# Optimization experiments

Measured on AMD Instinct MI355X. Metric: run time of the kernel, lower is better.

Reference implementation:

```python
import jax, jax.numpy as jnp
import numpy as np

DIM = 512   # feature channels (dim)
K = 3       # depthwise kernel size
H = 256     # grid extent along pos[:,0]
W = 256     # grid extent along pos[:,1]
N = 20000   # number of occupied spots (unique coordinates)


def setup_inputs() -> dict:
    key = jax.random.key(0)
    k1, k2, k3 = jax.random.split(key, 3)
    rng = np.random.default_rng(0)
    # N unique flat cells; pin corners so the dense grid extent is exactly HxW
    flat = np.concatenate([[0, H * W - 1], rng.permutation(H * W - 2)[: N - 2] + 1])
    pos = jnp.asarray(np.stack([flat // W, flat % W], axis=1), dtype=jnp.int32)  # (N,2)
    x = jax.random.normal(k1, (1, N, DIM), jnp.float32)
    weight = jax.random.normal(k2, (DIM, 1, K, K), jnp.float32) * 0.05  # depthwise OIHW
    bias = jax.random.normal(k3, (DIM,), jnp.float32) * 0.05
    return {"x": x, "pos": pos, "weight": weight, "bias": bias}


def reference(x, pos, weight, bias):
    pos = pos - pos.min(axis=0)                 # shift to origin (as torch)
    p0, p1 = pos[:, 0], pos[:, 1]
    xsq = x[0]                                  # (N, DIM)
    # scatter sparse coords to dense grid (duplicates would sum, coords unique)
    grid = jnp.zeros((H, W, DIM), x.dtype).at[p0, p1].add(xsq)   # (H, W, DIM)
    xd = grid.transpose(2, 1, 0)[None]          # (1, DIM, W, H) == permute(2,1,0).unsqueeze(0)
    conv = jax.lax.conv_general_dilated(
        xd, weight, (1, 1), "SAME",
        dimension_numbers=("NCHW", "OIHW", "NCHW"),
        feature_group_count=DIM,
    ) + bias[None, :, None, None]
    mask = xd.sum(axis=1, keepdims=True) != 0.0  # occupied cells
    out_d = jnp.where(mask, conv, 0.0) + xd      # masked residual
    dense = out_d[0].transpose(2, 1, 0)          # (H, W, DIM)
    # gather back to sparse values; torch to_sparse(2) orders rows lexicographically
    order = jnp.lexsort((p1, p0))
    vals = dense[p0[order], p1[order]]           # (N, DIM)
    return vals[None]                            # (1, N, DIM)
```

## Files before the change

### kernel.cpp

```cpp
#include <hip/hip_runtime.h>

#define HH 256
#define WW 256
#define DIM 512

typedef float f32x4 __attribute__((ext_vector_type(4)));


__global__ __launch_bounds__(256) void scatter_kernel(const int* __restrict__ pos,
                                                      int* __restrict__ cell_map,
                                                      int n) {
    int i = blockIdx.x * 256 + threadIdx.x;
    if (i >= n) return;
    int p0 = pos[2 * i];
    int p1 = pos[2 * i + 1];
    cell_map[p0 * WW + p1] = i;
}

__global__ __launch_bounds__(256) void rank_kernel(const int* __restrict__ cell_map,
                                                   int* __restrict__ sorted) {
    __shared__ int red[256];
    __shared__ int wt[4];
    const int t = threadIdx.x;
    const int b = blockIdx.x;
    const int limit = b * 256;

    int cnt = 0;
    const int4* cm4 = (const int4*)cell_map;
    for (int i = t; i * 4 < limit; i += 256) {
        int4 v = cm4[i];
        cnt += (v.x >= 0) + (v.y >= 0) + (v.z >= 0) + (v.w >= 0);
    }
    red[t] = cnt;
    __syncthreads();
    #pragma unroll
    for (int d = 128; d > 0; d >>= 1) {
        if (t < d) red[t] += red[t + d];
        __syncthreads();
    }
    int blk_off = red[0];

    int cell = limit + t;
    int m = cell_map[cell];
    bool occ = (m >= 0);
    unsigned long long mask = __ballot(occ);
    int lane = t & 63;
    int wave = t >> 6;
    int pre = __popcll(mask & ((1ull << lane) - 1ull));
    if (lane == 0) wt[wave] = __popcll(mask);
    __syncthreads();
    int woff = 0;
    for (int i = 0; i < wave; ++i) woff += wt[i];
    if (occ) sorted[blk_off + woff + pre] = (m << 16) | cell;
}

__global__ __launch_bounds__(256, 6) void conv_main(const float* __restrict__ x,
                                                    const float* __restrict__ weight,
                                                    const float* __restrict__ bias,
                                                    const int* __restrict__ cell_map,
                                                    const int* __restrict__ sorted,
                                                    float* __restrict__ out,
                                                    int n) {
    const int lane = threadIdx.x & 63;
    const int wv   = threadIdx.x >> 6;

    const int nb  = gridDim.x;
    const int cid = (blockIdx.x & 7) * (nb >> 3) + (blockIdx.x >> 3);
    const int T   = 2 * n;
    const int ppb = (T + nb - 1) / nb;
    const int base = cid * ppb;
    int endt = base + ppb; if (endt > T) endt = T;

    int t = base + wv;
    if (t >= endt) return;

    const int hf = t & 1;
    const int c0 = hf * (DIM / 2) + lane * 4;

    float wtv[36];
    {
        const float4* wb = (const float4*)(weight + c0 * 9);
        #pragma unroll
        for (int q = 0; q < 9; ++q) {
            float4 v = wb[q];
            wtv[4 * q + 0] = v.x; wtv[4 * q + 1] = v.y;
            wtv[4 * q + 2] = v.z; wtv[4 * q + 3] = v.w;
        }
    }
    float bj[4];
    {
        float4 b0 = *(const float4*)(bias + c0);
        bj[0]=b0.x; bj[1]=b0.y; bj[2]=b0.z; bj[3]=b0.w;
    }
    #pragma unroll
    for (int j = 0; j < 4; ++j) wtv[j * 9 + 4] += 1.0f;

    int pk = __builtin_amdgcn_readfirstlane(sorted[t >> 1]);

    while (t < endt) {
        const int tn = t + 4;
        int pk_next = 0;
        if (tn < endt)
            pk_next = __builtin_amdgcn_readfirstlane(sorted[tn >> 1]);

        const int p    = pk >> 16;
        const int flat = pk & 0xFFFF;
        const int h = flat >> 8;
        const int w = flat & (WW - 1);

        int m[9];
        #pragma unroll
        for (int k = 0; k < 9; ++k) {
            if (k == 4) { m[4] = -1; continue; }
            int dh = k % 3 - 1;
            int dw = k / 3 - 1;
            int hh = h + dh;
            int ww = w + dw;
            int v = -1;
            if ((unsigned)hh < (unsigned)HH && (unsigned)ww < (unsigned)WW)
                v = cell_map[hh * WW + ww];
            m[k] = __builtin_amdgcn_readfirstlane(v);
        }

        const float* xs = x + (size_t)p * DIM + c0;
        float4 s0 = *(const float4*)(xs);
        float acc[4];
        acc[0] = bj[0] + s0.x * wtv[0*9+4];
        acc[1] = bj[1] + s0.y * wtv[1*9+4];
        acc[2] = bj[2] + s0.z * wtv[2*9+4];
        acc[3] = bj[3] + s0.w * wtv[3*9+4];

        #pragma unroll
        for (int k = 0; k < 9; ++k) {
            if (k == 4) continue;
            if (m[k] >= 0) {
                const float* xn = x + (size_t)m[k] * DIM + c0;
                float4 n0 = *(const float4*)(xn);
                acc[0] += n0.x * wtv[0*9+k];
                acc[1] += n0.y * wtv[1*9+k];
                acc[2] += n0.z * wtv[2*9+k];
                acc[3] += n0.w * wtv[3*9+k];
            }
        }

        const int r = t >> 1;
        float* op = out + (size_t)r * DIM + c0;
        f32x4 o0 = { acc[0], acc[1], acc[2], acc[3] };
        __builtin_nontemporal_store(o0, (f32x4*)op);

        t = tn;
        pk = pk_next;
    }
}

extern "C" void kernel_launch(void* const* d_in, const int* in_sizes, int n_in,
                              void* d_out, int out_size, void* d_ws, size_t ws_size,
                              hipStream_t stream) {
    const float* x      = (const float*)d_in[0];
    const int*   pos    = (const int*)d_in[1];
    const float* weight = (const float*)d_in[2];
    const float* bias   = (const float*)d_in[3];
    float* out = (float*)d_out;

    int n = in_sizes[1] / 2;

    int* ws       = (int*)d_ws;
    int* cell_map = ws;
    int* sorted   = ws + HH * WW;

    scatter_kernel<<<(n + 255) / 256, 256, 0, stream>>>(pos, cell_map, n);
    rank_kernel<<<256, 256, 0, stream>>>(cell_map, sorted);

    const int nblocks = 1536;
    conv_main<<<nblocks, 256, 0, stream>>>(x, weight, bias, cell_map, sorted, out, n);
}
```

Before: 129.2 us.

## Software-pipeline neighbor lookup and use branchless zero-row loads in conv

The conv loop now resolves the next point's nine neighbor indices from cell_map while the current point's feature loads are in flight. It also replaces conditional neighbor loads with unconditional loads that point at a zeroed row, which scatter_kernel initialises in the workspace. Launch bounds go from 6 to 4 blocks per CU and the grid shrinks from 1536 to 1024 blocks to leave room for the extra registers. The cost is always issuing eight neighbor loads, including ones that only read zeros, plus more register pressure and lower occupancy.

```diff
diff --git a/kernel.cpp b/kernel.cpp
--- a/kernel.cpp
+++ b/kernel.cpp
@@ -9,7 +9,12 @@
 
 __global__ __launch_bounds__(256) void scatter_kernel(const int* __restrict__ pos,
                                                       int* __restrict__ cell_map,
+                                                      float* __restrict__ zrow,
                                                       int n) {
+    if (blockIdx.x == 0) {
+        float2 z = {0.0f, 0.0f};
+        ((float2*)zrow)[threadIdx.x] = z;
+    }
     int i = blockIdx.x * 256 + threadIdx.x;
     if (i >= n) return;
     int p0 = pos[2 * i];
@@ -54,20 +59,38 @@
     if (occ) sorted[blk_off + woff + pre] = (m << 16) | cell;
 }
 
-__global__ __launch_bounds__(256, 6) void conv_main(const float* __restrict__ x,
+__device__ __forceinline__ void resolve9(const int* __restrict__ cm, int pk, int* m) {
+    const int h = (pk >> 8) & 255;
+    const int w = pk & 255;
+    #pragma unroll
+    for (int k = 0; k < 9; ++k) {
+        if (k == 4) { m[4] = -1; continue; }
+        int dh = k % 3 - 1;
+        int dw = k / 3 - 1;
+        int hh = h + dh;
+        int ww = w + dw;
+        bool ok = ((hh | ww) & ~255) == 0;
+        int cl = ok ? hh * WW + ww : 0;
+        int v  = cm[cl];
+        m[k]   = ok ? v : -1;
+    }
+}
+
+__global__ __launch_bounds__(256, 4) void conv_main(const float* __restrict__ x,
                                                     const float* __restrict__ weight,
                                                     const float* __restrict__ bias,
                                                     const int* __restrict__ cell_map,
                                                     const int* __restrict__ sorted,
+                                                    const float* __restrict__ zrow,
                                                     float* __restrict__ out,
                                                     int n) {
     const int lane = threadIdx.x & 63;
     const int wv   = threadIdx.x >> 6;
 
-    const int nb  = gridDim.x;
-    const int cid = (blockIdx.x & 7) * (nb >> 3) + (blockIdx.x >> 3);
+    const int nbk = gridDim.x;
+    const int cid = (blockIdx.x & 7) * (nbk >> 3) + (blockIdx.x >> 3);
     const int T   = 2 * n;
-    const int ppb = (T + nb - 1) / nb;
+    const int ppb = (T + nbk - 1) / nbk;
     const int base = cid * ppb;
     int endt = base + ppb; if (endt > T) endt = T;
 
@@ -95,61 +118,55 @@
     #pragma unroll
     for (int j = 0; j < 4; ++j) wtv[j * 9 + 4] += 1.0f;
 
-    int pk = __builtin_amdgcn_readfirstlane(sorted[t >> 1]);
+    const float* xc = x + c0;
+    const float* zr = zrow + c0;
 
-    while (t < endt) {
-        const int tn = t + 4;
-        int pk_next = 0;
-        if (tn < endt)
-            pk_next = __builtin_amdgcn_readfirstlane(sorted[tn >> 1]);
+    int pk = sorted[t >> 1];
+    int tn = t + 4;
+    int pk_n = (tn < endt) ? sorted[tn >> 1] : pk;
 
-        const int p    = pk >> 16;
-        const int flat = pk & 0xFFFF;
-        const int h = flat >> 8;
-        const int w = flat & (WW - 1);
+    int m[9];
+    resolve9(cell_map, pk, m);
 
-        int m[9];
-        #pragma unroll
-        for (int k = 0; k < 9; ++k) {
-            if (k == 4) { m[4] = -1; continue; }
-            int dh = k % 3 - 1;
-            int dw = k / 3 - 1;
-            int hh = h + dh;
-            int ww = w + dw;
-            int v = -1;
-            if ((unsigned)hh < (unsigned)HH && (unsigned)ww < (unsigned)WW)
-                v = cell_map[hh * WW + ww];
-            m[k] = __builtin_amdgcn_readfirstlane(v);
-        }
+    while (true) {
+        const int p = pk >> 16;
 
-        const float* xs = x + (size_t)p * DIM + c0;
-        float4 s0 = *(const float4*)(xs);
-        float acc[4];
-        acc[0] = bj[0] + s0.x * wtv[0*9+4];
-        acc[1] = bj[1] + s0.y * wtv[1*9+4];
-        acc[2] = bj[2] + s0.z * wtv[2*9+4];
-        acc[3] = bj[3] + s0.w * wtv[3*9+4];
-
+        const float4 s = *(const float4*)(xc + (size_t)p * DIM);
+        float4 nbv[9];
         #pragma unroll
         for (int k = 0; k < 9; ++k) {
             if (k == 4) continue;
-            if (m[k] >= 0) {
-                const float* xn = x + (size_t)m[k] * DIM + c0;
-                float4 n0 = *(const float4*)(xn);
-                acc[0] += n0.x * wtv[0*9+k];
-                acc[1] += n0.y * wtv[1*9+k];
-                acc[2] += n0.z * wtv[2*9+k];
-                acc[3] += n0.w * wtv[3*9+k];
-            }
+            const float* xn = (m[k] >= 0) ? (xc + (size_t)m[k] * DIM) : zr;
+            nbv[k] = *(const float4*)xn;
         }
 
-        const int r = t >> 1;
-        float* op = out + (size_t)r * DIM + c0;
-        f32x4 o0 = { acc[0], acc[1], acc[2], acc[3] };
-        __builtin_nontemporal_store(o0, (f32x4*)op);
+        int m_n[9];
+        resolve9(cell_map, pk_n, m_n);
+
+        float a0 = bj[0] + s.x * wtv[0*9+4];
+        float a1 = bj[1] + s.y * wtv[1*9+4];
+        float a2 = bj[2] + s.z * wtv[2*9+4];
+        float a3 = bj[3] + s.w * wtv[3*9+4];
+        #pragma unroll
+        for (int k = 0; k < 9; ++k) {
+            if (k == 4) continue;
+            a0 += nbv[k].x * wtv[0*9+k];
+            a1 += nbv[k].y * wtv[1*9+k];
+            a2 += nbv[k].z * wtv[2*9+k];
+            a3 += nbv[k].w * wtv[3*9+k];
+        }
+
+        float* op = out + (size_t)(t >> 1) * DIM + c0;
+        f32x4 o = { a0, a1, a2, a3 };
+        __builtin_nontemporal_store(o, (f32x4*)op);
 
         t = tn;
-        pk = pk_next;
+        if (t >= endt) break;
+        tn = t + 4;
+        pk = pk_n;
+        pk_n = (tn < endt) ? sorted[tn >> 1] : pk_n;
+        #pragma unroll
+        for (int k = 0; k < 9; ++k) m[k] = m_n[k];
     }
 }
 
@@ -167,10 +184,11 @@
     int* ws       = (int*)d_ws;
     int* cell_map = ws;
     int* sorted   = ws + HH * WW;
+    float* zrow   = (float*)(ws + HH * WW + n);
 
-    scatter_kernel<<<(n + 255) / 256, 256, 0, stream>>>(pos, cell_map, n);
+    scatter_kernel<<<(n + 255) / 256, 256, 0, stream>>>(pos, cell_map, zrow, n);
     rank_kernel<<<256, 256, 0, stream>>>(cell_map, sorted);
 
-    const int nblocks = 1536;
-    conv_main<<<nblocks, 256, 0, stream>>>(x, weight, bias, cell_map, sorted, out, n);
+    const int nblocks = 1024;
+    conv_main<<<nblocks, 256, 0, stream>>>(x, weight, bias, cell_map, sorted, zrow, out, n);
 }
```

Result: no change. 131.2 us (+1.5%).

## Replace per-point gather conv with spatially tiled LDS-staged convolution

Applied to the files above, without the earlier changes.

The conv kernel is restructured from walking sorted points and gathering up to nine neighbour rows from global memory per output to processing 8x8 spatial tiles with a halo. Each block loads a 10x10x64-channel halo tile into shared memory once and computes all occupied cells from LDS, so each input row is read about once instead of up to nine times. The rank kernel now writes an inverse rank map instead of a sorted list, and the scatter kernel also transposes the weights to channel-contiguous layout. The cost is scalar (non-vector) global loads, a tile grid that covers all 65536 cells even though only about 30% are occupied, and more blocks.

```diff
diff --git a/kernel.cpp b/kernel.cpp
--- a/kernel.cpp
+++ b/kernel.cpp
@@ -3,14 +3,24 @@
 #define HH 256
 #define WW 256
 #define DIM 512
+#define TS 8
+#define HS 10
+#define CH 64
+#define NTILE 32
 
 typedef float f32x4 __attribute__((ext_vector_type(4)));
 
 
 __global__ __launch_bounds__(256) void scatter_kernel(const int* __restrict__ pos,
+                                                      const float* __restrict__ weight,
                                                       int* __restrict__ cell_map,
+                                                      float* __restrict__ wt_t,
                                                       int n) {
     int i = blockIdx.x * 256 + threadIdx.x;
+    if (i < 9 * DIM) {
+        int c = i / 9, k = i % 9;
+        wt_t[k * DIM + c] = weight[i];
+    }
     if (i >= n) return;
     int p0 = pos[2 * i];
     int p1 = pos[2 * i + 1];
@@ -18,7 +28,7 @@
 }
 
 __global__ __launch_bounds__(256) void rank_kernel(const int* __restrict__ cell_map,
-                                                   int* __restrict__ sorted) {
+                                                   int* __restrict__ inv_rank) {
     __shared__ int red[256];
     __shared__ int wt[4];
     const int t = threadIdx.x;
@@ -51,105 +61,72 @@
     __syncthreads();
     int woff = 0;
     for (int i = 0; i < wave; ++i) woff += wt[i];
-    if (occ) sorted[blk_off + woff + pre] = (m << 16) | cell;
+    if (occ) inv_rank[cell] = blk_off + woff + pre;
 }
 
-__global__ __launch_bounds__(256, 6) void conv_main(const float* __restrict__ x,
-                                                    const float* __restrict__ weight,
-                                                    const float* __restrict__ bias,
-                                                    const int* __restrict__ cell_map,
-                                                    const int* __restrict__ sorted,
-                                                    float* __restrict__ out,
-                                                    int n) {
-    const int lane = threadIdx.x & 63;
-    const int wv   = threadIdx.x >> 6;
+__global__ __launch_bounds__(256) void conv_tiled(const float* __restrict__ x,
+                                                  const float* __restrict__ wt_t,
+                                                  const float* __restrict__ bias,
+                                                  const int* __restrict__ cell_map,
+                                                  const int* __restrict__ inv_rank,
+                                                  float* __restrict__ out) {
+    __shared__ float xs[HS * HS][CH];
+    __shared__ int   ms[HS * HS];
 
-    const int nb  = gridDim.x;
-    const int cid = (blockIdx.x & 7) * (nb >> 3) + (blockIdx.x >> 3);
-    const int T   = 2 * n;
-    const int ppb = (T + nb - 1) / nb;
-    const int base = cid * ppb;
-    int endt = base + ppb; if (endt > T) endt = T;
+    const int tid  = threadIdx.x;
+    const int lane = tid & 63;
+    const int wv   = tid >> 6;
 
-    int t = base + wv;
-    if (t >= endt) return;
+    const int bid  = blockIdx.x;
+    const int loc  = bid >> 3;
+    const int tile = (bid & 7) * 128 + (loc >> 3);
+    const int c0   = (loc & 7) * CH;
+    const int ty   = tile >> 5;
+    const int tx   = tile & 31;
+    const int h0   = ty * TS - 1;
+    const int w0   = tx * TS - 1;
 
-    const int hf = t & 1;
-    const int c0 = hf * (DIM / 2) + lane * 4;
+    float wt[9];
+    #pragma unroll
+    for (int k = 0; k < 9; ++k) wt[k] = wt_t[k * DIM + c0 + lane];
+    wt[4] += 1.0f;
+    const float bs = bias[c0 + lane];
 
-    float wtv[36];
-    {
-        const float4* wb = (const float4*)(weight + c0 * 9);
-        #pragma unroll
-        for (int q = 0; q < 9; ++q) {
-            float4 v = wb[q];
-            wtv[4 * q + 0] = v.x; wtv[4 * q + 1] = v.y;
-            wtv[4 * q + 2] = v.z; wtv[4 * q + 3] = v.w;
-        }
+    if (tid < HS * HS) {
+        int hh = h0 + tid / HS;
+        int ww = w0 + tid % HS;
+        int m = -1;
+        if ((unsigned)hh < (unsigned)HH && (unsigned)ww < (unsigned)WW)
+            m = cell_map[hh * WW + ww];
+        ms[tid] = m;
     }
-    float bj[4];
-    {
-        float4 b0 = *(const float4*)(bias + c0);
-        bj[0]=b0.x; bj[1]=b0.y; bj[2]=b0.z; bj[3]=b0.w;
+    __syncthreads();
+
+    for (int idx = wv; idx < HS * HS; idx += 4) {
+        int m = ms[idx];
+        float v = 0.0f;
+        if (m >= 0) v = x[(size_t)m * DIM + c0 + lane];
+        xs[idx][lane] = v;
     }
-    #pragma unroll
-    for (int j = 0; j < 4; ++j) wtv[j * 9 + 4] += 1.0f;
+    __syncthreads();
 
-    int pk = __builtin_amdgcn_readfirstlane(sorted[t >> 1]);
-
-    while (t < endt) {
-        const int tn = t + 4;
-        int pk_next = 0;
-        if (tn < endt)
-            pk_next = __builtin_amdgcn_readfirstlane(sorted[tn >> 1]);
-
-        const int p    = pk >> 16;
-        const int flat = pk & 0xFFFF;
-        const int h = flat >> 8;
-        const int w = flat & (WW - 1);
-
-        int m[9];
+    #pragma unroll 4
+    for (int i = 0; i < 16; ++i) {
+        int ci = wv * 16 + i;
+        int ih = ci >> 3, iw = ci & 7;
+        int li = (ih + 1) * HS + (iw + 1);
+        int m = ms[li];
+        if (m < 0) continue;
+        int cell = (h0 + 1 + ih) * WW + (w0 + 1 + iw);
+        int r = inv_rank[cell];
+        float a = bs;
         #pragma unroll
         for (int k = 0; k < 9; ++k) {
-            if (k == 4) { m[4] = -1; continue; }
             int dh = k % 3 - 1;
             int dw = k / 3 - 1;
-            int hh = h + dh;
-            int ww = w + dw;
-            int v = -1;
-            if ((unsigned)hh < (unsigned)HH && (unsigned)ww < (unsigned)WW)
-                v = cell_map[hh * WW + ww];
-            m[k] = __builtin_amdgcn_readfirstlane(v);
+            a += xs[li + dh * HS + dw][lane] * wt[k];
         }
-
-        const float* xs = x + (size_t)p * DIM + c0;
-        float4 s0 = *(const float4*)(xs);
-        float acc[4];
-        acc[0] = bj[0] + s0.x * wtv[0*9+4];
-        acc[1] = bj[1] + s0.y * wtv[1*9+4];
-        acc[2] = bj[2] + s0.z * wtv[2*9+4];
-        acc[3] = bj[3] + s0.w * wtv[3*9+4];
-
-        #pragma unroll
-        for (int k = 0; k < 9; ++k) {
-            if (k == 4) continue;
-            if (m[k] >= 0) {
-                const float* xn = x + (size_t)m[k] * DIM + c0;
-                float4 n0 = *(const float4*)(xn);
-                acc[0] += n0.x * wtv[0*9+k];
-                acc[1] += n0.y * wtv[1*9+k];
-                acc[2] += n0.z * wtv[2*9+k];
-                acc[3] += n0.w * wtv[3*9+k];
-            }
-        }
-
-        const int r = t >> 1;
-        float* op = out + (size_t)r * DIM + c0;
-        f32x4 o0 = { acc[0], acc[1], acc[2], acc[3] };
-        __builtin_nontemporal_store(o0, (f32x4*)op);
-
-        t = tn;
-        pk = pk_next;
+        __builtin_nontemporal_store(a, &out[(size_t)r * DIM + c0 + lane]);
     }
 }
 
@@ -164,13 +141,14 @@
 
     int n = in_sizes[1] / 2;
 
-    int* ws       = (int*)d_ws;
-    int* cell_map = ws;
-    int* sorted   = ws + HH * WW;
+    int* ws        = (int*)d_ws;
+    int* cell_map  = ws;
+    int* inv_rank  = ws + HH * WW;
+    float* wt_t    = (float*)(ws + 2 * HH * WW);
 
-    scatter_kernel<<<(n + 255) / 256, 256, 0, stream>>>(pos, cell_map, n);
-    rank_kernel<<<256, 256, 0, stream>>>(cell_map, sorted);
+    scatter_kernel<<<(n + 255) / 256, 256, 0, stream>>>(pos, weight, cell_map, wt_t, n);
+    rank_kernel<<<256, 256, 0, stream>>>(cell_map, inv_rank);
 
-    const int nblocks = 1536;
-    conv_main<<<nblocks, 256, 0, stream>>>(x, weight, bias, cell_map, sorted, out, n);
+    const int nblocks = NTILE * NTILE * (DIM / CH);
+    conv_tiled<<<nblocks, 256, 0, stream>>>(x, wt_t, bias, cell_map, inv_rank, out);
 }
```

After: 138.3 us. +7.1%, slower.
